# Kernel optimization log

Measured on AMD Instinct MI355X. Metric: run time of the kernel, lower is better.

The kernel has to match this reference:

```python
import jax, jax.numpy as jnp
import numpy as np

B, T, C_FEAT, H = 1024, 256, 512, 256


def setup_inputs() -> dict:
    key = jax.random.key(0)
    ks = jax.random.split(key, 8)
    s_ih = 1.0 / np.sqrt(H)
    return {
        "features": jax.random.normal(ks[0], (B, T, C_FEAT), dtype=jnp.float32),
        "last_coord": jax.random.normal(ks[1], (B, 2), dtype=jnp.float32),
        "W_ih": jax.random.uniform(ks[2], (3 * H, C_FEAT + 2), jnp.float32, -s_ih, s_ih),
        "W_hh": jax.random.uniform(ks[3], (3 * H, H), jnp.float32, -s_ih, s_ih),
        "b_ih": jax.random.uniform(ks[4], (3 * H,), jnp.float32, -s_ih, s_ih),
        "b_hh": jax.random.uniform(ks[5], (3 * H,), jnp.float32, -s_ih, s_ih),
        "W_proj": jax.random.uniform(ks[6], (2, H), jnp.float32, -s_ih, s_ih),
        "b_proj": jax.random.uniform(ks[7], (2,), jnp.float32, -s_ih, s_ih),
    }


def reference(features, last_coord, W_ih, W_hh, b_ih, b_hh, W_proj, b_proj):
    # features: (B, T, C_feat); last_coord: (B, 2)
    Bb, Tt, Cf = features.shape
    Hh = W_hh.shape[1]
    h0 = jnp.zeros((Bb, Hh), dtype=features.dtype)

    def step(carry, feat_t):
        h, coord = carry
        x = jnp.concatenate([feat_t, coord], axis=1)          # (B, C+2)
        gi = x @ W_ih.T + b_ih                                 # (B, 3H)
        gh = h @ W_hh.T + b_hh                                 # (B, 3H)
        i_r, i_z, i_n = jnp.split(gi, 3, axis=1)
        h_r, h_z, h_n = jnp.split(gh, 3, axis=1)
        r = jax.nn.sigmoid(i_r + h_r)
        z = jax.nn.sigmoid(i_z + h_z)
        n = jnp.tanh(i_n + r * h_n)
        h_new = (1.0 - z) * n + z * h                          # PyTorch GRU update
        disp = h_new @ W_proj.T + b_proj                       # (B, 2)
        return (h_new, coord + disp), disp

    feats_t = jnp.swapaxes(features, 0, 1)                     # (T, B, C)
    _, disps = jax.lax.scan(step, (h0, last_coord), feats_t)   # (T, B, 2)
    return jnp.swapaxes(disps, 0, 1)                           # (B, T, 2)
```

## Files before the change

### kernel.cpp

```cpp
#include <hip/hip_runtime.h>
#include <stdint.h>

typedef unsigned short u16;
typedef unsigned int   u32;
typedef __attribute__((ext_vector_type(8))) __bf16 bf16x8;
typedef __attribute__((ext_vector_type(4))) float  f32x4;
typedef __attribute__((ext_vector_type(8))) u16    u16x8;
typedef __attribute__((ext_vector_type(4))) u16    u16x4;
typedef __attribute__((ext_vector_type(2))) u32    u32x2;
typedef __attribute__((ext_vector_type(2))) float  f32x2;

__device__ __forceinline__ u16 f2bf(float f) {
    u32 u = __float_as_uint(f);
    u32 r = (u + 0x7fffu + ((u >> 16) & 1u)) >> 16;
    return (u16)r;
}
__device__ __forceinline__ float bf2f(u16 v) { return __uint_as_float(((u32)v) << 16); }
__device__ __forceinline__ void gload_lds16(const void* g, void* l) {
    __builtin_amdgcn_global_load_lds((const __attribute__((address_space(1))) void*)g,
                                     (__attribute__((address_space(3))) void*)l, 16, 0, 0);
}

__global__ void k_prep(const float* __restrict__ W_ih, const float* __restrict__ W_hh,
                       const float* __restrict__ b_ih, const float* __restrict__ b_hh,
                       u16* __restrict__ Wf, u16* __restrict__ Whh, float* __restrict__ bsum) {
    int i = blockIdx.x * 256 + threadIdx.x;
    if (i < 768 * 512) { int o = i >> 9, k = i & 511; Wf[i] = f2bf(W_ih[o * 514 + k]); }
    if (i < 768 * 256) { Whh[i] = f2bf(W_hh[i]); }
    if (i < 768)       { bsum[i] = b_ih[i] + (i < 512 ? b_hh[i] : 0.f); }
}

__global__ void k_cast(const float* __restrict__ f, u16* __restrict__ o) {
    const size_t N8 = (size_t)262144 * 512 / 8;
    for (size_t i = (size_t)blockIdx.x * 256 + threadIdx.x; i < N8; i += (size_t)gridDim.x * 256) {
        float4 a = ((const float4*)f)[i * 2];
        float4 b = ((const float4*)f)[i * 2 + 1];
        u16x8 v;
        v[0] = f2bf(a.x); v[1] = f2bf(a.y); v[2] = f2bf(a.z); v[3] = f2bf(a.w);
        v[4] = f2bf(b.x); v[5] = f2bf(b.y); v[6] = f2bf(b.z); v[7] = f2bf(b.w);
        ((u16x8*)o)[i] = v;
    }
}

__device__ __forceinline__ void xcd_remap(int& n0, int& m0) {
    int phys = blockIdx.x + blockIdx.y * 6;
    int logical = (phys & 7) * 1536 + (phys >> 3);
    n0 = (logical % 6) * 128;
    m0 = (logical / 6) * 128;
}

__global__ __launch_bounds__(256) void k_gemm(const u16* __restrict__ featbf,
                                              const u16* __restrict__ Wf,
                                              const float* __restrict__ bsum,
                                              float* __restrict__ Gf) {
    __shared__ u16 As[128 * 64];
    __shared__ u16 Bs[128 * 64];
    const int tid = threadIdx.x;
    const int l = tid & 63, wv = tid >> 6;
    const int wr = wv >> 1, wc = wv & 1;
    const int lb = l & 15, lq = l >> 4;
    int n0, m0; xcd_remap(n0, m0);
    const int rl = l >> 3;
    const int c16 = (l & 7) * 16;
    const int sswz = (rl & 7) << 4;

    f32x4 acc[4][4] = {};

    for (int k0 = 0; k0 < 512; k0 += 64) {
        __syncthreads();
#pragma unroll
        for (int i = 0; i < 4; ++i) {
            int ci = wv * 4 + i;
            int r = ci * 8 + rl;
            const char* sa = (const char*)(featbf + (size_t)(m0 + r) * 512) + k0 * 2 + (c16 ^ sswz);
            gload_lds16(sa, (char*)As + ci * 1024);
            const char* sb = (const char*)(Wf + (size_t)(n0 + r) * 512) + k0 * 2 + (c16 ^ sswz);
            gload_lds16(sb, (char*)Bs + ci * 1024);
        }
        __syncthreads();
#pragma unroll
        for (int kc = 0; kc < 2; ++kc) {
            bf16x8 af[4], bfr[4];
#pragma unroll
            for (int mi = 0; mi < 4; ++mi) {
                int row = wr * 64 + mi * 16 + lb;
                af[mi] = *(const bf16x8*)((char*)As + row * 128 + (((kc * 32 + lq * 8) * 2) ^ ((row & 7) << 4)));
            }
#pragma unroll
            for (int ni = 0; ni < 4; ++ni) {
                int row = wc * 64 + ni * 16 + lb;
                bfr[ni] = *(const bf16x8*)((char*)Bs + row * 128 + (((kc * 32 + lq * 8) * 2) ^ ((row & 7) << 4)));
            }
#pragma unroll
            for (int mi = 0; mi < 4; ++mi)
#pragma unroll
                for (int ni = 0; ni < 4; ++ni)
                    acc[mi][ni] = __builtin_amdgcn_mfma_f32_16x16x32_bf16(af[mi], bfr[ni], acc[mi][ni], 0, 0, 0);
        }
    }
#pragma unroll
    for (int ni = 0; ni < 4; ++ni) {
        int o = n0 + wc * 64 + ni * 16 + lb;
        float bi = bsum[o];
#pragma unroll
        for (int mi = 0; mi < 4; ++mi) {
#pragma unroll
            for (int j = 0; j < 4; ++j) {
                int m = m0 + wr * 64 + mi * 16 + lq * 4 + j;
                int bb = m >> 8, tt = m & 255;
                Gf[(size_t)((tt << 10) + bb) * 768 + o] = acc[mi][ni][j] + bi;
            }
        }
    }
}

template<typename ST>
__global__ __launch_bounds__(256) void k_gemm_legacy(const float* __restrict__ feat,
                                                     const u16* __restrict__ Wf,
                                                     const float* __restrict__ bsum,
                                                     ST* __restrict__ Gf) {
    __shared__ u16 As[128 * 64];
    __shared__ u16 Bs[128 * 64];
    const int tid = threadIdx.x;
    const int l = tid & 63, wv = tid >> 6;
    const int wr = wv >> 1, wc = wv & 1;
    const int lb = l & 15, lq = l >> 4;
    int n0, m0; xcd_remap(n0, m0);
    const int srow = tid >> 1, scol = (tid & 1) * 32;

    f32x4 acc[4][4] = {};

    for (int k0 = 0; k0 < 512; k0 += 64) {
        __syncthreads();
        const float* ga = feat + (size_t)(m0 + srow) * 512 + k0 + scol;
        const u16*   gb = Wf + (n0 + srow) * 512 + k0 + scol;
        char* arow = (char*)As + srow * 128;
        char* brow = (char*)Bs + srow * 128;
        const int swz = (srow & 7) << 4;
#pragma unroll
        for (int i = 0; i < 4; ++i) {
            float4 f0 = *(const float4*)(ga + i * 8);
            float4 f1 = *(const float4*)(ga + i * 8 + 4);
            u16x8 v;
            v[0] = f2bf(f0.x); v[1] = f2bf(f0.y); v[2] = f2bf(f0.z); v[3] = f2bf(f0.w);
            v[4] = f2bf(f1.x); v[5] = f2bf(f1.y); v[6] = f2bf(f1.z); v[7] = f2bf(f1.w);
            *(u16x8*)(arow + (((scol + i * 8) * 2) ^ swz)) = v;
            u16x8 w8 = *(const u16x8*)(gb + i * 8);
            *(u16x8*)(brow + (((scol + i * 8) * 2) ^ swz)) = w8;
        }
        __syncthreads();
#pragma unroll
        for (int kc = 0; kc < 2; ++kc) {
            bf16x8 af[4], bfr[4];
#pragma unroll
            for (int mi = 0; mi < 4; ++mi) {
                int row = wr * 64 + mi * 16 + lb;
                af[mi] = *(const bf16x8*)((char*)As + row * 128 + (((kc * 32 + lq * 8) * 2) ^ ((row & 7) << 4)));
            }
#pragma unroll
            for (int ni = 0; ni < 4; ++ni) {
                int row = wc * 64 + ni * 16 + lb;
                bfr[ni] = *(const bf16x8*)((char*)Bs + row * 128 + (((kc * 32 + lq * 8) * 2) ^ ((row & 7) << 4)));
            }
#pragma unroll
            for (int mi = 0; mi < 4; ++mi)
#pragma unroll
                for (int ni = 0; ni < 4; ++ni)
                    acc[mi][ni] = __builtin_amdgcn_mfma_f32_16x16x32_bf16(af[mi], bfr[ni], acc[mi][ni], 0, 0, 0);
        }
    }
#pragma unroll
    for (int ni = 0; ni < 4; ++ni) {
        int o = n0 + wc * 64 + ni * 16 + lb;
        float bi = bsum[o];
#pragma unroll
        for (int mi = 0; mi < 4; ++mi) {
#pragma unroll
            for (int j = 0; j < 4; ++j) {
                int m = m0 + wr * 64 + mi * 16 + lq * 4 + j;
                int bb = m >> 8, tt = m & 255;
                size_t idx = (size_t)((tt << 10) + bb) * 768 + o;
                float v = acc[mi][ni][j] + bi;
                if constexpr (sizeof(ST) == 4) Gf[idx] = v; else Gf[idx] = f2bf(v);
            }
        }
    }
}

template<typename ST>
__global__ __launch_bounds__(512, 2) void k_rnn(const float* __restrict__ lastc,
                                                const float* __restrict__ W_ih,
                                                const float* __restrict__ bhh_g,
                                                const float* __restrict__ Wp,
                                                const float* __restrict__ bp,
                                                const u16* __restrict__ Whh,
                                                const ST* __restrict__ Gf,
                                                float* __restrict__ out) {
    __shared__ u16 Wlds[96 * 512];
    __shared__ u16 hbf[2][16 * 256];
    __shared__ f32x2 wcxyL[768];
    __shared__ float wpL[256 * 2];
    __shared__ float dPart[16][2][8];

    const int tid = threadIdx.x, l = tid & 63, wv = tid >> 6;
    const int lb = l & 15, lq = l >> 4;
    const int bb = blockIdx.x << 4;
    const int swz = (lb & 7) << 4;

    bf16x8 wres[6][3][2];
    float bhhn[2][4];
#pragma unroll
    for (int g = 0; g < 3; ++g)
#pragma unroll
        for (int ut = 0; ut < 2; ++ut) {
            int row = g * 256 + (2 * wv + ut) * 16 + lb;
#pragma unroll
            for (int kc = 0; kc < 6; ++kc)
                wres[kc][g][ut] = *(const bf16x8*)(Whh + row * 256 + kc * 32 + lq * 8);
        }
#pragma unroll
    for (int ut = 0; ut < 2; ++ut)
#pragma unroll
        for (int j = 0; j < 4; ++j)
            bhhn[ut][j] = bhh_g[512 + (2 * wv + ut) * 16 + lq * 4 + j];

    for (int i = tid; i < 24576; i += 512) {
        int s = i >> 8, r = i & 255, ll = r >> 2, e = r & 3;
        int g = s >> 5, rem = s & 31, tt = rem >> 1, kcs = rem & 1;
        int row = g * 256 + tt * 16 + (ll & 15);
        int k = (6 + kcs) * 32 + (ll >> 4) * 8 + e * 2;
        ((u32*)Wlds)[i] = *(const u32*)(Whh + row * 256 + k);
    }
    for (int i = tid; i < 2 * 16 * 256 / 2; i += 512) ((u32*)hbf)[i] = 0u;
    for (int i = tid; i < 768; i += 512) {
        f32x2 w; w.x = W_ih[i * 514 + 512]; w.y = W_ih[i * 514 + 513];
        wcxyL[i] = w;
    }
    if (tid < 256) { wpL[tid * 2] = Wp[tid]; wpL[tid * 2 + 1] = Wp[256 + tid]; }
    const float bp0 = bp[0], bp1 = bp[1];
    float cx = lastc[(bb + lb) * 2], cy = lastc[(bb + lb) * 2 + 1];
    __syncthreads();

    float hreg[2][4] = {};
    float prevD0 = 0.f, prevD1 = 0.f;
    const ST* gr = Gf + (size_t)(bb + lb) * 768 + lq * 4;
    int par = 0;

    for (int t = 0; t < 256; ++t) {
        if (t > 0 && wv == 0 && lq == 0) {
            f32x2 d; d.x = prevD0; d.y = prevD1;
            *(f32x2*)(out + ((size_t)(bb + lb) * 256 + (t - 1)) * 2) = d;
        }

        float gf[3][2][4];
#pragma unroll
        for (int g = 0; g < 3; ++g)
#pragma unroll
            for (int ut = 0; ut < 2; ++ut) {
                int off = g * 256 + (2 * wv + ut) * 16;
                if constexpr (sizeof(ST) == 4) {
                    float4 v = *(const float4*)(gr + off);
                    gf[g][ut][0] = v.x; gf[g][ut][1] = v.y; gf[g][ut][2] = v.z; gf[g][ut][3] = v.w;
                } else {
                    u16x4 v = *(const u16x4*)(gr + off);
#pragma unroll
                    for (int j = 0; j < 4; ++j) gf[g][ut][j] = bf2f(v[j]);
                }
            }

        const char* hrow = (const char*)hbf + par * 8192 + lb * 512;
        f32x4 acc[3][2] = {};
#pragma unroll
        for (int kc = 0; kc < 6; ++kc) {
            bf16x8 hb = *(const bf16x8*)(hrow + ((kc * 64 + lq * 16) ^ swz));
#pragma unroll
            for (int g = 0; g < 3; ++g)
#pragma unroll
                for (int ut = 0; ut < 2; ++ut)
                    acc[g][ut] = __builtin_amdgcn_mfma_f32_16x16x32_bf16(wres[kc][g][ut], hb, acc[g][ut], 0, 0, 0);
        }
#pragma unroll
        for (int kcs = 0; kcs < 2; ++kcs) {
            bf16x8 hb = *(const bf16x8*)(hrow + (((6 + kcs) * 64 + lq * 16) ^ swz));
#pragma unroll
            for (int g = 0; g < 3; ++g)
#pragma unroll
                for (int ut = 0; ut < 2; ++ut) {
                    int s = (g * 16 + (2 * wv + ut)) * 2 + kcs;
                    bf16x8 wl = *(const bf16x8*)((const char*)Wlds + s * 1024 + l * 16);
                    acc[g][ut] = __builtin_amdgcn_mfma_f32_16x16x32_bf16(wl, hb, acc[g][ut], 0, 0, 0);
                }
        }

        char* hwr = (char*)hbf + (par ^ 1) * 8192 + lb * 512;
        float pd0 = 0.f, pd1 = 0.f;
#pragma unroll
        for (int ut = 0; ut < 2; ++ut) {
            int row0 = (2 * wv + ut) * 16 + lq * 4;
            int ub = row0;
            float4 wpa = *(const float4*)(wpL + ub * 2);
            float4 wpb = *(const float4*)(wpL + ub * 2 + 4);
            float4 cr0 = *(const float4*)(&wcxyL[row0]);
            float4 cr1 = *(const float4*)(&wcxyL[row0 + 2]);
            float4 cz0 = *(const float4*)(&wcxyL[256 + row0]);
            float4 cz1 = *(const float4*)(&wcxyL[256 + row0 + 2]);
            float4 cn0 = *(const float4*)(&wcxyL[512 + row0]);
            float4 cn1 = *(const float4*)(&wcxyL[512 + row0 + 2]);
            float ctr[4] = { cr0.x * cx + cr0.y * cy, cr0.z * cx + cr0.w * cy,
                             cr1.x * cx + cr1.y * cy, cr1.z * cx + cr1.w * cy };
            float ctz[4] = { cz0.x * cx + cz0.y * cy, cz0.z * cx + cz0.w * cy,
                             cz1.x * cx + cz1.y * cy, cz1.z * cx + cz1.w * cy };
            float ctn[4] = { cn0.x * cx + cn0.y * cy, cn0.z * cx + cn0.w * cy,
                             cn1.x * cx + cn1.y * cy, cn1.z * cx + cn1.w * cy };
            u16 hpk[4];
#pragma unroll
            for (int j = 0; j < 4; ++j) {
                float r = 1.f / (1.f + __expf(-(gf[0][ut][j] + ctr[j] + acc[0][ut][j])));
                float z = 1.f / (1.f + __expf(-(gf[1][ut][j] + ctz[j] + acc[1][ut][j])));
                float ghn = acc[2][ut][j] + bhhn[ut][j];
                float xn = gf[2][ut][j] + ctn[j] + r * ghn;
                float e = __expf(-2.f * fabsf(xn));
                float th = (1.f - e) / (1.f + e);
                th = (xn >= 0.f) ? th : -th;
                float hn = (1.f - z) * th + z * hreg[ut][j];
                hreg[ut][j] = hn;
                float w0 = (j == 0) ? wpa.x : (j == 1) ? wpa.z : (j == 2) ? wpb.x : wpb.z;
                float w1 = (j == 0) ? wpa.y : (j == 1) ? wpa.w : (j == 2) ? wpb.y : wpb.w;
                pd0 += w0 * hn;
                pd1 += w1 * hn;
                hpk[j] = f2bf(hn);
            }
            u32x2 pv;
            pv.x = (u32)hpk[0] | ((u32)hpk[1] << 16);
            pv.y = (u32)hpk[2] | ((u32)hpk[3] << 16);
            *(u32x2*)(hwr + ((ub * 2) ^ swz)) = pv;
        }
        pd0 += __shfl_xor(pd0, 16); pd0 += __shfl_xor(pd0, 32);
        pd1 += __shfl_xor(pd1, 16); pd1 += __shfl_xor(pd1, 32);
        if (l < 16) { dPart[l][0][wv] = pd0; dPart[l][1][wv] = pd1; }
        __syncthreads();

        {
            float4 a0 = *(const float4*)(&dPart[lb][0][0]);
            float4 a1 = *(const float4*)(&dPart[lb][0][4]);
            float4 b0 = *(const float4*)(&dPart[lb][1][0]);
            float4 b1 = *(const float4*)(&dPart[lb][1][4]);
            float d0 = bp0 + a0.x + a0.y + a0.z + a0.w + a1.x + a1.y + a1.z + a1.w;
            float d1 = bp1 + b0.x + b0.y + b0.z + b0.w + b1.x + b1.y + b1.z + b1.w;
            cx += d0; cy += d1;
            prevD0 = d0; prevD1 = d1;
        }
        __syncthreads();
        par ^= 1;
        gr += (size_t)1024 * 768;
    }
    if (wv == 0 && lq == 0) {
        f32x2 d; d.x = prevD0; d.y = prevD1;
        *(f32x2*)(out + ((size_t)(bb + lb) * 256 + 255) * 2) = d;
    }
}

extern "C" void kernel_launch(void* const* d_in, const int* in_sizes, int n_in,
                              void* d_out, int out_size, void* d_ws, size_t ws_size,
                              hipStream_t stream) {
    const float* feat   = (const float*)d_in[0];
    const float* lastc  = (const float*)d_in[1];
    const float* W_ih   = (const float*)d_in[2];
    const float* W_hh   = (const float*)d_in[3];
    const float* b_ih   = (const float*)d_in[4];
    const float* b_hh   = (const float*)d_in[5];
    const float* W_proj = (const float*)d_in[6];
    const float* b_proj = (const float*)d_in[7];
    float* out = (float*)d_out;

    char* ws = (char*)d_ws;
    u16*   Wf    = (u16*)ws;
    u16*   Whh   = (u16*)(ws + 786432);
    float* bsum  = (float*)(ws + 786432 + 393216);
    const size_t off_fb = 786432 + 393216 + 3072;
    u16*   featbf = (u16*)(ws + off_fb);
    const size_t off_gf_full = off_fb + (size_t)262144 * 512 * 2;
    const size_t need_full  = off_gf_full + (size_t)262144 * 768 * 4;
    const size_t need_tier2 = off_fb + (size_t)262144 * 768 * 4;

    k_prep<<<1536, 256, 0, stream>>>(W_ih, W_hh, b_ih, b_hh, Wf, Whh, bsum);

    if (ws_size >= need_full) {
        float* Gf = (float*)(ws + off_gf_full);
        k_cast<<<16384, 256, 0, stream>>>(feat, featbf);
        k_gemm<<<dim3(6, 2048), 256, 0, stream>>>(featbf, Wf, bsum, Gf);
        k_rnn<float><<<64, 512, 0, stream>>>(lastc, W_ih, b_hh, W_proj, b_proj, Whh, Gf, out);
    } else if (ws_size >= need_tier2) {
        float* Gf = (float*)(ws + off_fb);
        k_gemm_legacy<float><<<dim3(6, 2048), 256, 0, stream>>>(feat, Wf, bsum, Gf);
        k_rnn<float><<<64, 512, 0, stream>>>(lastc, W_ih, b_hh, W_proj, b_proj, Whh, Gf, out);
    } else {
        u16* Gf = (u16*)(ws + off_fb);
        k_gemm_legacy<u16><<<dim3(6, 2048), 256, 0, stream>>>(feat, Wf, bsum, Gf);
        k_rnn<u16><<<64, 512, 0, stream>>>(lastc, W_ih, b_hh, W_proj, b_proj, Whh, Gf, out);
    }
}
```

Measured before the change: 1.603 ms.

## Rebalance W_hh between registers and LDS, single-buffer h, keep small weights in registers

Moves one more K-chunk of the recurrent weights from registers into LDS (5 register chunks, 3 LDS chunks) and uses the freed registers to hold the coordinate-input weights packed as bf16 pairs, the projection weights, and the n-gate bias. This removes the per-step LDS reads of wcxyL and wpL. The h buffer drops from double to single buffering: a barrier placed after the MFMAs replaces the end-of-step barrier, so the number of barriers per step stays the same. Trade-offs are more LDS traffic per step for the W_hh chunk and a small precision loss from rounding the coordinate weights to bf16.

```diff
diff --git a/kernel.cpp b/kernel.cpp
--- a/kernel.cpp
+++ b/kernel.cpp
@@ -16,6 +16,8 @@
     return (u16)r;
 }
 __device__ __forceinline__ float bf2f(u16 v) { return __uint_as_float(((u32)v) << 16); }
+__device__ __forceinline__ float bflo(u32 v) { return __uint_as_float(v << 16); }
+__device__ __forceinline__ float bfhi(u32 v) { return __uint_as_float(v & 0xffff0000u); }
 __device__ __forceinline__ void gload_lds16(const void* g, void* l) {
     __builtin_amdgcn_global_load_lds((const __attribute__((address_space(1))) void*)g,
                                      (__attribute__((address_space(3))) void*)l, 16, 0, 0);
@@ -196,47 +198,50 @@
                                                 const u16* __restrict__ Whh,
                                                 const ST* __restrict__ Gf,
                                                 float* __restrict__ out) {
-    __shared__ u16 Wlds[96 * 512];
-    __shared__ u16 hbf[2][16 * 256];
-    __shared__ f32x2 wcxyL[768];
-    __shared__ float wpL[256 * 2];
-    __shared__ float dPart[16][2][8];
+    __shared__ u16 Wlds[144 * 512];
+    __shared__ u16 hbf[16 * 256];
+    __shared__ float dPart[16][10][2];
 
     const int tid = threadIdx.x, l = tid & 63, wv = tid >> 6;
     const int lb = l & 15, lq = l >> 4;
     const int bb = blockIdx.x << 4;
     const int swz = (lb & 7) << 4;
 
-    bf16x8 wres[6][3][2];
-    float bhhn[2][4];
+    bf16x8 wres[5][3][2];
+    u32 cpk[3][2][4];
+    float bhhn[2][4], wp0[2][4], wp1[2][4];
 #pragma unroll
     for (int g = 0; g < 3; ++g)
 #pragma unroll
         for (int ut = 0; ut < 2; ++ut) {
             int row = g * 256 + (2 * wv + ut) * 16 + lb;
 #pragma unroll
-            for (int kc = 0; kc < 6; ++kc)
+            for (int kc = 0; kc < 5; ++kc)
                 wres[kc][g][ut] = *(const bf16x8*)(Whh + row * 256 + kc * 32 + lq * 8);
+#pragma unroll
+            for (int j = 0; j < 4; ++j) {
+                int rr = g * 256 + (2 * wv + ut) * 16 + lq * 4 + j;
+                cpk[g][ut][j] = (u32)f2bf(W_ih[rr * 514 + 512]) | ((u32)f2bf(W_ih[rr * 514 + 513]) << 16);
+            }
         }
 #pragma unroll
     for (int ut = 0; ut < 2; ++ut)
 #pragma unroll
-        for (int j = 0; j < 4; ++j)
-            bhhn[ut][j] = bhh_g[512 + (2 * wv + ut) * 16 + lq * 4 + j];
-
-    for (int i = tid; i < 24576; i += 512) {
-        int s = i >> 8, r = i & 255, ll = r >> 2, e = r & 3;
-        int g = s >> 5, rem = s & 31, tt = rem >> 1, kcs = rem & 1;
+        for (int j = 0; j < 4; ++j) {
+            int u = (2 * wv + ut) * 16 + lq * 4 + j;
+            bhhn[ut][j] = bhh_g[512 + u];
+            wp0[ut][j] = Wp[u];
+            wp1[ut][j] = Wp[256 + u];
+        }
+
+    for (int i = tid; i < 36864; i += 512) {
+        int s = i >> 8, r = i & 255, ll = r >> 2, e2 = r & 3;
+        int g = s / 48, rem = s - g * 48, tt = rem / 3, kcs = rem - tt * 3;
         int row = g * 256 + tt * 16 + (ll & 15);
-        int k = (6 + kcs) * 32 + (ll >> 4) * 8 + e * 2;
+        int k = (5 + kcs) * 32 + (ll >> 4) * 8 + e2 * 2;
         ((u32*)Wlds)[i] = *(const u32*)(Whh + row * 256 + k);
     }
-    for (int i = tid; i < 2 * 16 * 256 / 2; i += 512) ((u32*)hbf)[i] = 0u;
-    for (int i = tid; i < 768; i += 512) {
-        f32x2 w; w.x = W_ih[i * 514 + 512]; w.y = W_ih[i * 514 + 513];
-        wcxyL[i] = w;
-    }
-    if (tid < 256) { wpL[tid * 2] = Wp[tid]; wpL[tid * 2 + 1] = Wp[256 + tid]; }
+    for (int i = tid; i < 2048; i += 512) ((u32*)hbf)[i] = 0u;
     const float bp0 = bp[0], bp1 = bp[1];
     float cx = lastc[(bb + lb) * 2], cy = lastc[(bb + lb) * 2 + 1];
     __syncthreads();
@@ -244,7 +249,7 @@
     float hreg[2][4] = {};
     float prevD0 = 0.f, prevD1 = 0.f;
     const ST* gr = Gf + (size_t)(bb + lb) * 768 + lq * 4;
-    int par = 0;
+    const char* hrow = (const char*)hbf + lb * 512;
 
     for (int t = 0; t < 256; ++t) {
         if (t > 0 && wv == 0 && lq == 0) {
@@ -268,10 +273,9 @@
                 }
             }
 
-        const char* hrow = (const char*)hbf + par * 8192 + lb * 512;
         f32x4 acc[3][2] = {};
 #pragma unroll
-        for (int kc = 0; kc < 6; ++kc) {
+        for (int kc = 0; kc < 5; ++kc) {
             bf16x8 hb = *(const bf16x8*)(hrow + ((kc * 64 + lq * 16) ^ swz));
 #pragma unroll
             for (int g = 0; g < 3; ++g)
@@ -280,78 +284,66 @@
                     acc[g][ut] = __builtin_amdgcn_mfma_f32_16x16x32_bf16(wres[kc][g][ut], hb, acc[g][ut], 0, 0, 0);
         }
 #pragma unroll
-        for (int kcs = 0; kcs < 2; ++kcs) {
-            bf16x8 hb = *(const bf16x8*)(hrow + (((6 + kcs) * 64 + lq * 16) ^ swz));
+        for (int kcs = 0; kcs < 3; ++kcs) {
+            bf16x8 hb = *(const bf16x8*)(hrow + (((5 + kcs) * 64 + lq * 16) ^ swz));
 #pragma unroll
             for (int g = 0; g < 3; ++g)
 #pragma unroll
                 for (int ut = 0; ut < 2; ++ut) {
-                    int s = (g * 16 + (2 * wv + ut)) * 2 + kcs;
+                    int s = (g * 16 + 2 * wv + ut) * 3 + kcs;
                     bf16x8 wl = *(const bf16x8*)((const char*)Wlds + s * 1024 + l * 16);
                     acc[g][ut] = __builtin_amdgcn_mfma_f32_16x16x32_bf16(wl, hb, acc[g][ut], 0, 0, 0);
                 }
         }
-
-        char* hwr = (char*)hbf + (par ^ 1) * 8192 + lb * 512;
+        __syncthreads();
+
         float pd0 = 0.f, pd1 = 0.f;
 #pragma unroll
         for (int ut = 0; ut < 2; ++ut) {
-            int row0 = (2 * wv + ut) * 16 + lq * 4;
-            int ub = row0;
-            float4 wpa = *(const float4*)(wpL + ub * 2);
-            float4 wpb = *(const float4*)(wpL + ub * 2 + 4);
-            float4 cr0 = *(const float4*)(&wcxyL[row0]);
-            float4 cr1 = *(const float4*)(&wcxyL[row0 + 2]);
-            float4 cz0 = *(const float4*)(&wcxyL[256 + row0]);
-            float4 cz1 = *(const float4*)(&wcxyL[256 + row0 + 2]);
-            float4 cn0 = *(const float4*)(&wcxyL[512 + row0]);
-            float4 cn1 = *(const float4*)(&wcxyL[512 + row0 + 2]);
-            float ctr[4] = { cr0.x * cx + cr0.y * cy, cr0.z * cx + cr0.w * cy,
-                             cr1.x * cx + cr1.y * cy, cr1.z * cx + cr1.w * cy };
-            float ctz[4] = { cz0.x * cx + cz0.y * cy, cz0.z * cx + cz0.w * cy,
-                             cz1.x * cx + cz1.y * cy, cz1.z * cx + cz1.w * cy };
-            float ctn[4] = { cn0.x * cx + cn0.y * cy, cn0.z * cx + cn0.w * cy,
-                             cn1.x * cx + cn1.y * cy, cn1.z * cx + cn1.w * cy };
+            int ub = (2 * wv + ut) * 16 + lq * 4;
             u16 hpk[4];
 #pragma unroll
             for (int j = 0; j < 4; ++j) {
-                float r = 1.f / (1.f + __expf(-(gf[0][ut][j] + ctr[j] + acc[0][ut][j])));
-                float z = 1.f / (1.f + __expf(-(gf[1][ut][j] + ctz[j] + acc[1][ut][j])));
+                u32 cr = cpk[0][ut][j], cz = cpk[1][ut][j], cn = cpk[2][ut][j];
+                float ctr = bflo(cr) * cx + bfhi(cr) * cy;
+                float ctz = bflo(cz) * cx + bfhi(cz) * cy;
+                float ctn = bflo(cn) * cx + bfhi(cn) * cy;
+                float r = 1.f / (1.f + __expf(-(gf[0][ut][j] + ctr + acc[0][ut][j])));
+                float z = 1.f / (1.f + __expf(-(gf[1][ut][j] + ctz + acc[1][ut][j])));
                 float ghn = acc[2][ut][j] + bhhn[ut][j];
-                float xn = gf[2][ut][j] + ctn[j] + r * ghn;
+                float xn = gf[2][ut][j] + ctn + r * ghn;
                 float e = __expf(-2.f * fabsf(xn));
                 float th = (1.f - e) / (1.f + e);
                 th = (xn >= 0.f) ? th : -th;
                 float hn = (1.f - z) * th + z * hreg[ut][j];
                 hreg[ut][j] = hn;
-                float w0 = (j == 0) ? wpa.x : (j == 1) ? wpa.z : (j == 2) ? wpb.x : wpb.z;
-                float w1 = (j == 0) ? wpa.y : (j == 1) ? wpa.w : (j == 2) ? wpb.y : wpb.w;
-                pd0 += w0 * hn;
-                pd1 += w1 * hn;
+                pd0 += wp0[ut][j] * hn;
+                pd1 += wp1[ut][j] * hn;
                 hpk[j] = f2bf(hn);
             }
             u32x2 pv;
             pv.x = (u32)hpk[0] | ((u32)hpk[1] << 16);
             pv.y = (u32)hpk[2] | ((u32)hpk[3] << 16);
-            *(u32x2*)(hwr + ((ub * 2) ^ swz)) = pv;
+            *(u32x2*)((char*)hbf + lb * 512 + ((ub * 2) ^ swz)) = pv;
         }
         pd0 += __shfl_xor(pd0, 16); pd0 += __shfl_xor(pd0, 32);
         pd1 += __shfl_xor(pd1, 16); pd1 += __shfl_xor(pd1, 32);
-        if (l < 16) { dPart[l][0][wv] = pd0; dPart[l][1][wv] = pd1; }
+        if (l < 16) {
+            f32x2 d; d.x = pd0; d.y = pd1;
+            *(f32x2*)(&dPart[l][wv][0]) = d;
+        }
         __syncthreads();
 
         {
             float4 a0 = *(const float4*)(&dPart[lb][0][0]);
-            float4 a1 = *(const float4*)(&dPart[lb][0][4]);
-            float4 b0 = *(const float4*)(&dPart[lb][1][0]);
-            float4 b1 = *(const float4*)(&dPart[lb][1][4]);
-            float d0 = bp0 + a0.x + a0.y + a0.z + a0.w + a1.x + a1.y + a1.z + a1.w;
-            float d1 = bp1 + b0.x + b0.y + b0.z + b0.w + b1.x + b1.y + b1.z + b1.w;
+            float4 a1 = *(const float4*)(&dPart[lb][2][0]);
+            float4 a2 = *(const float4*)(&dPart[lb][4][0]);
+            float4 a3 = *(const float4*)(&dPart[lb][6][0]);
+            float d0 = bp0 + a0.x + a0.z + a1.x + a1.z + a2.x + a2.z + a3.x + a3.z;
+            float d1 = bp1 + a0.y + a0.w + a1.y + a1.w + a2.y + a2.w + a3.y + a3.w;
             cx += d0; cy += d1;
             prevD0 = d0; prevD1 = d1;
         }
-        __syncthreads();
-        par ^= 1;
         gr += (size_t)1024 * 768;
     }
     if (wv == 0 && lq == 0) {
```

Result: slower. 1.960 ms (+22.3%).
